# Kernel optimization log

Hardware: AMD Instinct MI355X
Metric: run time of the kernel (lower is better)

## Reference

```python
import jax, jax.numpy as jnp
import numpy as np

INPUT_DIM = 1024
DAY_EMB = 8
PRED_LEN = 96
HIDDEN = 512
BATCH = 4096


def setup_inputs() -> dict:
    key = jax.random.key(0)
    ks = jax.random.split(key, 6)
    x = jax.random.normal(ks[0], (BATCH, INPUT_DIM), dtype=jnp.float32)
    day_emb = jax.random.normal(ks[1], (PRED_LEN, DAY_EMB), dtype=jnp.float32)
    # stacked per-head first-layer weights: in = input_dim + day_emb_dim
    W1 = jax.random.normal(ks[2], (PRED_LEN, INPUT_DIM + DAY_EMB, HIDDEN), dtype=jnp.float32) * 0.02
    b1 = jax.random.normal(ks[3], (PRED_LEN, HIDDEN), dtype=jnp.float32) * 0.02
    # stacked per-head output Linear(hidden, 1) weights (squeezed)
    W2 = jax.random.normal(ks[4], (PRED_LEN, HIDDEN), dtype=jnp.float32) * 0.02
    b2 = jax.random.normal(ks[5], (PRED_LEN,), dtype=jnp.float32) * 0.02
    return {"x": x, "day_emb": day_emb, "W1": W1, "b1": b1, "W2": W2, "b2": b2}


def reference(x, day_emb, W1, b1, W2, b2):
    # Each head p sees f = concat([x, day_emb[p]]) -> Linear -> ReLU -> (Dropout eval=id) -> Linear(.,1)
    # Split W1 into the x-part and emb-part so we never materialize the [P,B,in+emb] concat.
    W1x = W1[:, :INPUT_DIM, :]          # [P, D, H]
    W1e = W1[:, INPUT_DIM:, :]          # [P, E, H]
    h = jnp.einsum('bd,pdh->pbh', x, W1x)  # [P, B, H]
    h = h + (jnp.einsum('pe,peh->ph', day_emb, W1e) + b1)[:, None, :]
    h = jax.nn.relu(h)
    out = jnp.einsum('pbh,ph->pb', h, W2) + b2[:, None]  # [P, B]
    return out.T  # [B, pred_len]
```

## Files before the change

kernel.cpp:

```cpp
#include <hip/hip_runtime.h>
#include <hip/hip_bf16.h>
#include <stdint.h>

#define INPUT_DIM 1024
#define PRED_LEN 96
#define HIDDEN 512
#define BATCH 4096
#define W1_ROWS 1032

typedef __attribute__((ext_vector_type(8))) short bf16x8;
typedef __attribute__((ext_vector_type(4))) float floatx4;

__device__ __forceinline__ unsigned short f32_to_bf16_rne(float f) {
    union { float f; unsigned int u; } v; v.f = f;
    unsigned int u = v.u;
    unsigned int r = u + 0x7fffu + ((u >> 16) & 1u);
    return (unsigned short)(r >> 16);
}

__device__ __forceinline__ unsigned int pack_bf16x2(float lo, float hi) {
    return (unsigned int)f32_to_bf16_rne(lo) | ((unsigned int)f32_to_bf16_rne(hi) << 16);
}

__device__ __forceinline__ void async_copy16(const void* g, void* l) {
    __builtin_amdgcn_global_load_lds(
        (const __attribute__((address_space(1))) unsigned int*)g,
        (__attribute__((address_space(3))) unsigned int*)l, 16, 0, 0);
}

#define TP_BLOCKS  (PRED_LEN * 8 * 4)
#define CV_BLOCKS  ((BATCH * INPUT_DIM) / (256 * 8))
__global__ void __launch_bounds__(256) prep_kernel(
        const float* __restrict__ x,
        const float* __restrict__ W1,
        const float* __restrict__ day_emb,
        const float* __restrict__ b1,
        unsigned short* __restrict__ xb,
        unsigned short* __restrict__ W1t,
        float* __restrict__ bias) {
    const int bid = blockIdx.x;
    const int t   = threadIdx.x;

    if (bid < TP_BLOCKS) {
        const int nt = bid & 7;
        const int kt = (bid >> 3) & 3;
        const int p  = bid >> 5;
        const int tn = t & 15;
        const int tk = t >> 4;
        const int n0 = nt * 64;
        const int k0 = kt * 256;

        const float* src = W1 + (size_t)p * W1_ROWS * HIDDEN
                              + (size_t)(k0 + 16 * tk) * HIDDEN + n0 + 4 * tn;
        float4 v[16];
        #pragma unroll
        for (int i = 0; i < 16; ++i)
            v[i] = *reinterpret_cast<const float4*>(src + (size_t)i * HIDDEN);

        size_t dst = ((size_t)p * HIDDEN + n0 + 4 * tn) * 1024 + k0 + 16 * tk;
        #pragma unroll
        for (int j = 0; j < 4; ++j) {
            float c[16];
            #pragma unroll
            for (int i = 0; i < 16; ++i)
                c[i] = (j == 0) ? v[i].x : (j == 1) ? v[i].y : (j == 2) ? v[i].z : v[i].w;
            uint4 o0, o1;
            o0.x = pack_bf16x2(c[0],  c[1]);
            o0.y = pack_bf16x2(c[2],  c[3]);
            o0.z = pack_bf16x2(c[4],  c[5]);
            o0.w = pack_bf16x2(c[6],  c[7]);
            o1.x = pack_bf16x2(c[8],  c[9]);
            o1.y = pack_bf16x2(c[10], c[11]);
            o1.z = pack_bf16x2(c[12], c[13]);
            o1.w = pack_bf16x2(c[14], c[15]);
            unsigned short* d = W1t + dst + (size_t)j * 1024;
            *reinterpret_cast<uint4*>(d)     = o0;
            *reinterpret_cast<uint4*>(d + 8) = o1;
        }
    } else if (bid < TP_BLOCKS + CV_BLOCKS) {
        const int b = bid - TP_BLOCKS;
        const int i = (b * 256 + t) * 8;
        float4 a = *reinterpret_cast<const float4*>(x + i);
        float4 c = *reinterpret_cast<const float4*>(x + i + 4);
        uint4 o;
        o.x = pack_bf16x2(a.x, a.y);
        o.y = pack_bf16x2(a.z, a.w);
        o.z = pack_bf16x2(c.x, c.y);
        o.w = pack_bf16x2(c.z, c.w);
        *reinterpret_cast<uint4*>(xb + i) = o;
    } else {
        const int p = bid - (TP_BLOCKS + CV_BLOCKS);
        const float* W1e = W1 + ((size_t)p * W1_ROWS + INPUT_DIM) * HIDDEN;
        #pragma unroll
        for (int s = 0; s < 2; ++s) {
            const int h = t + s * 256;
            float acc = b1[p * HIDDEN + h];
            #pragma unroll
            for (int e = 0; e < 8; ++e)
                acc += day_emb[p * 8 + e] * W1e[(size_t)e * HIDDEN + h];
            bias[p * HIDDEN + h] = acc;
        }
    }
}

__global__ void __launch_bounds__(256, 3)
mlp_head_kernel(const unsigned short* __restrict__ xb,
                const unsigned short* __restrict__ W1t,
                const float* __restrict__ bias,
                const float* __restrict__ W2,
                const float* __restrict__ b2,
                float* __restrict__ out)
{
    __shared__ unsigned short As[128 * 64];
    __shared__ unsigned short Bs[128 * 64];
    __shared__ float w2s[HIDDEN];
    __shared__ float biass[HIDDEN];
    __shared__ float red[2][128];

    const int mt   = blockIdx.x;
    const int p    = blockIdx.y;
    const int t    = threadIdx.x;
    const int lane = t & 63;
    const int w    = t >> 6;
    const int wi   = w >> 1;
    const int wj   = w & 1;
    const int l15  = lane & 15;
    const int quad = lane >> 4;
    const int xl   = l15 & 7;

    const int t3    = t >> 3;
    const int skc   = ((t & 7) ^ (t3 & 7)) * 8;
    const int ldsq8 = t * 8;

    for (int i = t; i < HIDDEN; i += 256) {
        w2s[i]   = W2[p * HIDDEN + i];
        biass[i] = bias[p * HIDDEN + i];
    }

    const int m0 = mt * 128;
    const unsigned short* ag = xb  + (size_t)m0 * 1024 + (size_t)t3 * 1024 + skc;
    const unsigned short* bg = W1t + (size_t)p * HIDDEN * 1024 + (size_t)t3 * 1024 + skc;

    float partial[4][4];
    #pragma unroll
    for (int i = 0; i < 4; ++i)
        #pragma unroll
        for (int r = 0; r < 4; ++r) partial[i][r] = 0.f;

    for (int nt = 0; nt < 4; ++nt) {
        floatx4 acc[4][4];
        #pragma unroll
        for (int i = 0; i < 4; ++i)
            #pragma unroll
            for (int j = 0; j < 4; ++j)
                acc[i][j] = (floatx4){0.f, 0.f, 0.f, 0.f};

        const size_t bn = (size_t)nt * 128 * 1024;

        for (int k0 = 0; k0 < 1024; k0 += 64) {
            __syncthreads();
            #pragma unroll
            for (int c = 0; c < 4; ++c) {
                async_copy16(ag + (size_t)c * 32 * 1024 + k0,      As + ldsq8 + c * 2048);
                async_copy16(bg + bn + (size_t)c * 32 * 1024 + k0, Bs + ldsq8 + c * 2048);
            }
            __syncthreads();
            #pragma unroll
            for (int kk = 0; kk < 2; ++kk) {
                const int slot = (kk * 4 + quad) ^ xl;
                bf16x8 af[4], bfr[4];
                #pragma unroll
                for (int i = 0; i < 4; ++i) {
                    int r = wi * 64 + i * 16 + l15;
                    af[i] = *reinterpret_cast<const bf16x8*>(As + r * 64 + slot * 8);
                }
                #pragma unroll
                for (int j = 0; j < 4; ++j) {
                    int n = wj * 64 + j * 16 + l15;
                    bfr[j] = *reinterpret_cast<const bf16x8*>(Bs + n * 64 + slot * 8);
                }
                #pragma unroll
                for (int i = 0; i < 4; ++i)
                    #pragma unroll
                    for (int j = 0; j < 4; ++j)
                        acc[i][j] = __builtin_amdgcn_mfma_f32_16x16x32_bf16(
                            af[i], bfr[j], acc[i][j], 0, 0, 0);
            }
        }

        const int n0 = nt * 128;
        #pragma unroll
        for (int j = 0; j < 4; ++j) {
            int c = n0 + wj * 64 + j * 16 + l15;
            float w2v = w2s[c];
            float bv  = biass[c];
            #pragma unroll
            for (int i = 0; i < 4; ++i)
                #pragma unroll
                for (int r = 0; r < 4; ++r) {
                    float hv = acc[i][j][r] + bv;
                    hv = hv > 0.f ? hv : 0.f;
                    partial[i][r] += hv * w2v;
                }
        }
    }

    #pragma unroll
    for (int i = 0; i < 4; ++i)
        #pragma unroll
        for (int r = 0; r < 4; ++r) {
            float v = partial[i][r];
            v += __shfl_xor(v, 1);
            v += __shfl_xor(v, 2);
            v += __shfl_xor(v, 4);
            v += __shfl_xor(v, 8);
            partial[i][r] = v;
        }

    if (l15 == 0) {
        #pragma unroll
        for (int i = 0; i < 4; ++i)
            #pragma unroll
            for (int r = 0; r < 4; ++r) {
                int row = wi * 64 + i * 16 + quad * 4 + r;
                red[wj][row] = partial[i][r];
            }
    }
    __syncthreads();
    if (t < 128) {
        float v = red[0][t] + red[1][t] + b2[p];
        out[(size_t)(m0 + t) * PRED_LEN + p] = v;
    }
}

extern "C" void kernel_launch(void* const* d_in, const int* in_sizes, int n_in,
                              void* d_out, int out_size, void* d_ws, size_t ws_size,
                              hipStream_t stream) {
    const float* x       = (const float*)d_in[0];
    const float* day_emb = (const float*)d_in[1];
    const float* W1      = (const float*)d_in[2];
    const float* b1      = (const float*)d_in[3];
    const float* W2      = (const float*)d_in[4];
    const float* b2      = (const float*)d_in[5];
    float* out = (float*)d_out;

    const size_t xb_bytes  = (size_t)BATCH * INPUT_DIM * 2;
    const size_t w1t_bytes = (size_t)PRED_LEN * HIDDEN * INPUT_DIM * 2;
    const size_t bias_bytes = (size_t)PRED_LEN * HIDDEN * 4;
    if (ws_size < xb_bytes + w1t_bytes + bias_bytes) return;

    unsigned short* xb  = (unsigned short*)d_ws;
    unsigned short* w1t = (unsigned short*)((char*)d_ws + xb_bytes);
    float* biasp        = (float*)((char*)d_ws + xb_bytes + w1t_bytes);

    prep_kernel<<<TP_BLOCKS + CV_BLOCKS + PRED_LEN, 256, 0, stream>>>(
        x, W1, day_emb, b1, xb, w1t, biasp);

    dim3 grid(BATCH / 128, PRED_LEN);
    mlp_head_kernel<<<grid, 256, 0, stream>>>(xb, w1t, biasp, W2, b2, out);
}
```

Before: 667.5 us.

## Double-buffer LDS tiles and flatten N/K loops into one pipelined loop

```diff
diff --git a/kernel.cpp b/kernel.cpp
--- a/kernel.cpp
+++ b/kernel.cpp
@@ -103,7 +103,7 @@
     }
 }
 
-__global__ void __launch_bounds__(256, 3)
+__global__ void __launch_bounds__(256, 2)
 mlp_head_kernel(const unsigned short* __restrict__ xb,
                 const unsigned short* __restrict__ W1t,
                 const float* __restrict__ bias,
@@ -111,8 +111,8 @@
                 const float* __restrict__ b2,
                 float* __restrict__ out)
 {
-    __shared__ unsigned short As[128 * 64];
-    __shared__ unsigned short Bs[128 * 64];
+    __shared__ unsigned short As[2][128 * 64];
+    __shared__ unsigned short Bs[2][128 * 64];
     __shared__ float w2s[HIDDEN];
     __shared__ float biass[HIDDEN];
     __shared__ float red[2][128];
@@ -136,6 +136,7 @@
         w2s[i]   = W2[p * HIDDEN + i];
         biass[i] = bias[p * HIDDEN + i];
     }
+    __syncthreads();
 
     const int m0 = mt * 128;
     const unsigned short* ag = xb  + (size_t)m0 * 1024 + (size_t)t3 * 1024 + skc;
@@ -147,62 +148,86 @@
         #pragma unroll
         for (int r = 0; r < 4; ++r) partial[i][r] = 0.f;
 
-    for (int nt = 0; nt < 4; ++nt) {
-        floatx4 acc[4][4];
-        #pragma unroll
-        for (int i = 0; i < 4; ++i)
-            #pragma unroll
-            for (int j = 0; j < 4; ++j)
-                acc[i][j] = (floatx4){0.f, 0.f, 0.f, 0.f};
-
-        const size_t bn = (size_t)nt * 128 * 1024;
-
-        for (int k0 = 0; k0 < 1024; k0 += 64) {
-            __syncthreads();
+    floatx4 acc[4][4];
+    #pragma unroll
+    for (int i = 0; i < 4; ++i)
+        #pragma unroll
+        for (int j = 0; j < 4; ++j)
+            acc[i][j] = (floatx4){0.f, 0.f, 0.f, 0.f};
+
+    #pragma unroll
+    for (int c = 0; c < 4; ++c) {
+        async_copy16(ag + (size_t)c * 32768,      &As[0][ldsq8 + c * 2048]);
+        async_copy16(bg + (size_t)c * 32768,      &Bs[0][ldsq8 + c * 2048]);
+    }
+
+    #pragma unroll 1
+    for (int vk = 0; vk < 64; ++vk) {
+        const int cur = vk & 1;
+
+        if (vk < 63) {
+            const int nvk   = vk + 1;
+            const int k0n   = (nvk & 15) << 6;
+            const size_t bnn = (size_t)(nvk >> 4) * 131072;
+            unsigned short* Ad = &As[cur ^ 1][ldsq8];
+            unsigned short* Bd = &Bs[cur ^ 1][ldsq8];
             #pragma unroll
             for (int c = 0; c < 4; ++c) {
-                async_copy16(ag + (size_t)c * 32 * 1024 + k0,      As + ldsq8 + c * 2048);
-                async_copy16(bg + bn + (size_t)c * 32 * 1024 + k0, Bs + ldsq8 + c * 2048);
-            }
-            __syncthreads();
-            #pragma unroll
-            for (int kk = 0; kk < 2; ++kk) {
-                const int slot = (kk * 4 + quad) ^ xl;
-                bf16x8 af[4], bfr[4];
+                async_copy16(ag + (size_t)c * 32768 + k0n,       Ad + c * 2048);
+                async_copy16(bg + bnn + (size_t)c * 32768 + k0n, Bd + c * 2048);
+            }
+            asm volatile("s_waitcnt vmcnt(8)" ::: "memory");
+        } else {
+            asm volatile("s_waitcnt vmcnt(0)" ::: "memory");
+        }
+        __builtin_amdgcn_s_barrier();
+        asm volatile("" ::: "memory");
+
+        const unsigned short* Ab = &As[cur][0];
+        const unsigned short* Bb = &Bs[cur][0];
+        #pragma unroll
+        for (int kk = 0; kk < 2; ++kk) {
+            const int slot = (kk * 4 + quad) ^ xl;
+            bf16x8 af[4], bfr[4];
+            #pragma unroll
+            for (int i = 0; i < 4; ++i) {
+                int r = wi * 64 + i * 16 + l15;
+                af[i] = *reinterpret_cast<const bf16x8*>(Ab + r * 64 + slot * 8);
+            }
+            #pragma unroll
+            for (int j = 0; j < 4; ++j) {
+                int n = wj * 64 + j * 16 + l15;
+                bfr[j] = *reinterpret_cast<const bf16x8*>(Bb + n * 64 + slot * 8);
+            }
+            #pragma unroll
+            for (int i = 0; i < 4; ++i)
                 #pragma unroll
-                for (int i = 0; i < 4; ++i) {
-                    int r = wi * 64 + i * 16 + l15;
-                    af[i] = *reinterpret_cast<const bf16x8*>(As + r * 64 + slot * 8);
-                }
-                #pragma unroll
-                for (int j = 0; j < 4; ++j) {
-                    int n = wj * 64 + j * 16 + l15;
-                    bfr[j] = *reinterpret_cast<const bf16x8*>(Bs + n * 64 + slot * 8);
-                }
+                for (int j = 0; j < 4; ++j)
+                    acc[i][j] = __builtin_amdgcn_mfma_f32_16x16x32_bf16(
+                        af[i], bfr[j], acc[i][j], 0, 0, 0);
+        }
+
+        if ((vk & 15) == 15) {
+            const int n0 = (vk >> 4) * 128;
+            #pragma unroll
+            for (int j = 0; j < 4; ++j) {
+                int c = n0 + wj * 64 + j * 16 + l15;
+                float w2v = w2s[c];
+                float bv  = biass[c];
                 #pragma unroll
                 for (int i = 0; i < 4; ++i)
                     #pragma unroll
-                    for (int j = 0; j < 4; ++j)
-                        acc[i][j] = __builtin_amdgcn_mfma_f32_16x16x32_bf16(
-                            af[i], bfr[j], acc[i][j], 0, 0, 0);
-            }
-        }
-
-        const int n0 = nt * 128;
-        #pragma unroll
-        for (int j = 0; j < 4; ++j) {
-            int c = n0 + wj * 64 + j * 16 + l15;
-            float w2v = w2s[c];
-            float bv  = biass[c];
-            #pragma unroll
-            for (int i = 0; i < 4; ++i)
-                #pragma unroll
-                for (int r = 0; r < 4; ++r) {
-                    float hv = acc[i][j][r] + bv;
-                    hv = hv > 0.f ? hv : 0.f;
-                    partial[i][r] += hv * w2v;
-                }
-        }
+                    for (int r = 0; r < 4; ++r) {
+                        float hv = acc[i][j][r] + bv;
+                        hv = hv > 0.f ? hv : 0.f;
+                        partial[i][r] += hv * w2v;
+                        acc[i][j][r] = 0.f;
+                    }
+            }
+        }
+
+        asm volatile("" ::: "memory");
+        __builtin_amdgcn_s_barrier();
     }
 
     #pragma unroll
```

Result: slower. 735.2 us (+10.1%).
